# Performance work log

Hardware: AMD Instinct MI355X
Metric: run time of the kernel (lower is better)

Reference implementation:

```python
import jax, jax.numpy as jnp
import numpy as np


def _conv(x, w, b):
    # stride-2, pad-1 3x3 conv, NCHW/OIHW
    y = jax.lax.conv_general_dilated(x, w, (2, 2), [(1, 1), (1, 1)],
                                     dimension_numbers=('NCHW', 'OIHW', 'NCHW'))
    return y + b[None, :, None, None]


def _bn(x, g, b, eps=1e-5):
    # BatchNorm2d in training mode: batch statistics over (N, H, W)
    m = x.mean((0, 2, 3), keepdims=True)
    v = x.var((0, 2, 3), keepdims=True)
    return (x - m) * jax.lax.rsqrt(v + eps) * g[None, :, None, None] + b[None, :, None, None]


def setup_inputs() -> dict:
    key = jax.random.key(0)
    ks = iter(jax.random.split(key, 64))
    def rn(shape, scale):
        return jax.random.normal(next(ks), shape, jnp.float32) * scale
    d = {}
    d['img'] = jax.random.normal(next(ks), (64, 3, 128, 128), jnp.float32)
    d['qst'] = jax.random.normal(next(ks), (64, 11), jnp.float32)
    cin = 3
    for i in range(1, 5):
        d[f'cw{i}'] = rn((24, cin, 3, 3), 1.0 / np.sqrt(cin * 9))
        d[f'cb{i}'] = jnp.zeros((24,), jnp.float32)
        d[f'bg{i}'] = jnp.ones((24,), jnp.float32)
        d[f'bb{i}'] = jnp.zeros((24,), jnp.float32)
        cin = 24
    gdims = [63, 256, 256, 256]
    for i in range(1, 5):
        d[f'gw{i}'] = rn((gdims[i - 1], 256), 1.0 / np.sqrt(gdims[i - 1]))
        d[f'gb{i}'] = jnp.zeros((256,), jnp.float32)
    fdims = [(256, 256), (256, 256), (256, 10)]
    for i, (a, b) in enumerate(fdims, 1):
        d[f'fw{i}'] = rn((a, b), 1.0 / np.sqrt(a))
        d[f'fb{i}'] = jnp.zeros((b,), jnp.float32)
    return d


def reference(img, qst,
              cw1, cb1, bg1, bb1, cw2, cb2, bg2, bb2,
              cw3, cb3, bg3, bb3, cw4, cb4, bg4, bb4,
              gw1, gb1, gw2, gb2, gw3, gb3, gw4, gb4,
              fw1, fb1, fw2, fb2, fw3, fb3):
    x = img
    for cw, cb, bg, bb in ((cw1, cb1, bg1, bb1), (cw2, cb2, bg2, bb2),
                           (cw3, cb3, bg3, bb3), (cw4, cb4, bg4, bb4)):
        x = _bn(jax.nn.relu(_conv(x, cw, cb)), bg, bb)
    B, C, H, W = x.shape
    n = H * W  # number of objects (feature-map cells)
    o = x.reshape(B, C, n).transpose(0, 2, 1)  # [B, n, 24]
    idx = jnp.arange(n)
    coords = jnp.stack([idx // H, idx % W], axis=1).astype(x.dtype)  # [n, 2]
    o = jnp.concatenate([o, jnp.broadcast_to(coords, (B, n, 2))], axis=2)  # [B, n, 26]
    # First G layer fused over the pairwise concat cat([x_i, x_j, qst], -1) @ gw1:
    # x_i[b,a,c] = o[b,c], x_j[b,a,c] = o[b,a] -> split gw1 into the three blocks.
    Wi, Wj, Wq = gw1[:26], gw1[26:52], gw1[52:]
    h = jax.nn.relu((o @ Wi)[:, None, :, :]
                    + (o @ Wj)[:, :, None, :]
                    + (qst @ Wq + gb1)[:, None, None, :])  # [B, n, n, 256]
    h = jax.nn.relu(h @ gw2 + gb2)
    h = jax.nn.relu(h @ gw3 + gb3)
    h = jax.nn.relu(h @ gw4 + gb4)
    g = h.sum((1, 2))  # sum over all n*n pairs -> [B, 256]
    f = jax.nn.relu(g @ fw1 + fb1)
    f = jax.nn.relu(f @ fw2 + fb2)  # Dropout(0.5) is identity at inference
    return jax.nn.softmax(f @ fw3 + fb3, axis=-1)
```

## Files before the change

kernel.cpp:

```cpp
#include <hip/hip_runtime.h>
#include <hip/hip_bf16.h>

typedef __attribute__((ext_vector_type(8))) short bf16x8_t;
typedef __attribute__((ext_vector_type(4))) float f32x4_t;

__device__ __forceinline__ unsigned bfr(float x) {
  unsigned u = __builtin_bit_cast(unsigned, x);
  return (u + 0x7fffu + ((u >> 16) & 1u)) >> 16;
}
__device__ __forceinline__ unsigned pk2(float lo, float hi) {
  return bfr(lo) | (bfr(hi) << 16);
}

template<int CIN, int H, int COG, bool BNIN>
__global__ __launch_bounds__(256) void convk(
    const float* __restrict__ x, const float* __restrict__ wgt,
    const float* __restrict__ bias,
    const float* __restrict__ instats,
    const float* __restrict__ ing, const float* __restrict__ inb,
    float* __restrict__ y, float* __restrict__ stats)
{
  constexpr int W = H, HO = H / 2, WO = W / 2;
  constexpr int PXB = (COG == 1) ? 256 : 64;
  constexpr int OHS = PXB / WO;
  constexpr int SPB = HO / OHS;
  constexpr int NR = 2 * OHS + 1;
  constexpr int TW = W + 1;
  constexpr int NSTG = NR * W;
  constexpr int NCO = 24 / COG;

  __shared__ float tile[2][NR][TW];
  __shared__ float scb[CIN], shb[CIN];
  __shared__ float sred[24], sqd[24];

  const int tid = threadIdx.x;
  const int b = blockIdx.x / SPB;
  const int strip = blockIdx.x % SPB;
  const int oh0 = strip * OHS;
  const int lane = tid & 63;

  if (BNIN && tid < CIN) {
    const float cnt = 64.f * H * W;
    const float m = instats[tid] / cnt;
    const float v = instats[24 + tid] / cnt - m * m;
    const float s = rsqrtf(v + 1e-5f) * ing[tid];
    scb[tid] = s;
    shb[tid] = inb[tid] - m * s;
  }
  if (tid < 24) { sred[tid] = 0.f; sqd[tid] = 0.f; }
  for (int i = tid; i < 2 * NR; i += 256)
    tile[i / NR][i % NR][0] = 0.f;
  __syncthreads();

  const int px = (COG == 1) ? tid : lane;
  const int ow = px % WO;
  const int ohl = px / WO;
  const int oh = oh0 + ohl;
  const int cb = (COG == 1) ? 0
               : __builtin_amdgcn_readfirstlane(tid >> 6) * NCO;

  float acc[NCO];
  #pragma unroll
  for (int n = 0; n < NCO; ++n) acc[n] = bias[cb + n];

  {
    const float sc = BNIN ? scb[0] : 1.f, sh = BNIN ? shb[0] : 0.f;
    #pragma unroll
    for (int idx = tid; idx < NSTG; idx += 256) {
      const int c = idx % W, rl = idx / W;
      const int ih = oh0 * 2 - 1 + rl;
      float v = 0.f;
      if (ih >= 0)
        v = x[((size_t)(b * CIN + 0) * H + ih) * W + c] * sc + sh;
      tile[0][rl][c + 1] = v;
    }
  }
  __syncthreads();

  for (int ci = 0; ci < CIN; ++ci) {
    if (ci + 1 < CIN) {
      const float sc = BNIN ? scb[ci + 1] : 1.f, sh = BNIN ? shb[ci + 1] : 0.f;
      #pragma unroll
      for (int idx = tid; idx < NSTG; idx += 256) {
        const int c = idx % W, rl = idx / W;
        const int ih = oh0 * 2 - 1 + rl;
        float v = 0.f;
        if (ih >= 0)
          v = x[((size_t)(b * CIN + ci + 1) * H + ih) * W + c] * sc + sh;
        tile[(ci + 1) & 1][rl][c + 1] = v;
      }
    }
    float tp[9];
    #pragma unroll
    for (int r = 0; r < 3; ++r)
      #pragma unroll
      for (int s = 0; s < 3; ++s)
        tp[r * 3 + s] = tile[ci & 1][2 * ohl + r][2 * ow + s];
    #pragma unroll
    for (int n = 0; n < NCO; ++n) {
      const float* wp = wgt + (size_t)((cb + n) * CIN + ci) * 9;
      float a = acc[n];
      #pragma unroll
      for (int k = 0; k < 9; ++k) a += tp[k] * wp[k];
      acc[n] = a;
    }
    __syncthreads();
  }

  #pragma unroll
  for (int n = 0; n < NCO; ++n) {
    const float v = fmaxf(acc[n], 0.f);
    acc[n] = v;
    y[((size_t)(b * 24 + cb + n) * HO + oh) * WO + ow] = v;
  }
  #pragma unroll
  for (int n = 0; n < NCO; ++n) {
    float v = acc[n], q = v * v;
    #pragma unroll
    for (int d = 1; d < 64; d <<= 1) {
      v += __shfl_xor(v, d, 64);
      q += __shfl_xor(q, d, 64);
    }
    if (lane == 0) {
      atomicAdd(&sred[cb + n], v);
      atomicAdd(&sqd[cb + n], q);
    }
  }
  __syncthreads();
  if (tid < 24) {
    atomicAdd(&stats[tid], sred[tid]);
    atomicAdd(&stats[24 + tid], sqd[tid]);
  }
}

__global__ __launch_bounds__(256) void build_ab(
    const float* __restrict__ x4, const float* __restrict__ stats4,
    const float* __restrict__ g4, const float* __restrict__ b4,
    const float* __restrict__ gw1, const float* __restrict__ gb1,
    const float* __restrict__ qst,
    float* __restrict__ A, float* __restrict__ Bm, float* __restrict__ Cq)
{
  const int bp = blockIdx.x;
  const int b = bp >> 3, pg = bp & 7;
  const int t = threadIdx.x;
  __shared__ float o[8][26];
  if (t < 208) {
    const int r = t / 26, c = t % 26;
    if (c < 24) {
      const float m = stats4[c] * (1.f / 4096.f);
      const float v = stats4[24 + c] * (1.f / 4096.f) - m * m;
      const float sc = rsqrtf(v + 1e-5f) * g4[c];
      const float sh = b4[c] - m * sc;
      o[r][c] = x4[(size_t)(b * 24 + c) * 64 + pg * 8 + r] * sc + sh;
    } else if (c == 24) o[r][24] = (float)pg;
    else                o[r][25] = (float)r;
  }
  __syncthreads();
  float accA[8], accB[8];
  #pragma unroll
  for (int r = 0; r < 8; ++r) { accA[r] = 0.f; accB[r] = 0.f; }
  #pragma unroll
  for (int c = 0; c < 26; ++c) {
    const float wi = gw1[c * 256 + t];
    const float wj = gw1[(26 + c) * 256 + t];
    #pragma unroll
    for (int r = 0; r < 8; ++r) {
      accA[r] += o[r][c] * wi;
      accB[r] += o[r][c] * wj;
    }
  }
  #pragma unroll
  for (int r = 0; r < 8; ++r) {
    A[(size_t)(b * 64 + pg * 8 + r) * 256 + t]  = accA[r];
    Bm[(size_t)(b * 64 + pg * 8 + r) * 256 + t] = accB[r];
  }
  if (pg == 0) {
    float cqa = gb1[t];
    #pragma unroll
    for (int c = 0; c < 11; ++c)
      cqa += qst[b * 11 + c] * gw1[(52 + c) * 256 + t];
    Cq[b * 256 + t] = cqa;
  }
}

__global__ __launch_bounds__(256) void wt_convert_frag(
    const float* __restrict__ W2, const float* __restrict__ W3,
    const float* __restrict__ W4, unsigned short* __restrict__ wt)
{
  const int c = blockIdx.x;
  const int layer = c >> 3, ks = c & 7;
  const float* W = layer == 0 ? W2 : layer == 1 ? W3 : W4;
  const int t = threadIdx.x;
  #pragma unroll
  for (int q = 0; q < 4; ++q) {
    const int f = q * 256 + t;
    const int cg = f >> 8, a = (f >> 6) & 3, ln = f & 63;
    const int n = cg * 64 + a * 16 + (ln & 15);
    const int k0 = ks * 32 + (ln >> 4) * 8;
    float w[8];
    #pragma unroll
    for (int u = 0; u < 8; ++u) w[u] = W[(size_t)(k0 + u) * 256 + n];
    uint4 ov;
    ov.x = pk2(w[0], w[1]); ov.y = pk2(w[2], w[3]);
    ov.z = pk2(w[4], w[5]); ov.w = pk2(w[6], w[7]);
    *(uint4*)(wt + (size_t)c * 8192 + (size_t)f * 8) = ov;
  }
}

__global__ __launch_bounds__(256) void pair_mfma(
    const float* __restrict__ A, const float* __restrict__ Bm,
    const float* __restrict__ Cq,
    const unsigned short* __restrict__ wtall,
    const float* __restrict__ b2, const float* __restrict__ b3,
    const float* __restrict__ b4,
    float* __restrict__ Gpart)
{
  __shared__ __align__(16) unsigned short hsm[64 * 256];
  __shared__ __align__(16) unsigned short wbuf[2][8192];
  __shared__ float gpart[256];

  const int tid = threadIdx.x;
  int bid = blockIdx.x;
  bid = (bid & 7) * 512 + (bid >> 3);
  const int b = bid >> 6, local = bid & 63;
  const int lane = tid & 63, cg = tid >> 6;
  const int l15 = lane & 15, l4 = lane >> 4;
  char* hbase = (char*)hsm;

  {
    const int m = tid >> 2, seg = tid & 3;
    const float* Ar = A  + (size_t)(b * 64 + m) * 256 + seg * 64;
    const float* Br = Bm + (size_t)(b * 64 + local) * 256 + seg * 64;
    const float* Cr = Cq + (size_t)b * 256 + seg * 64;
    #pragma unroll
    for (int it = 0; it < 8; ++it) {
      const float4 a0 = *(const float4*)(Ar + it * 8);
      const float4 a1 = *(const float4*)(Ar + it * 8 + 4);
      const float4 b0 = *(const float4*)(Br + it * 8);
      const float4 b1 = *(const float4*)(Br + it * 8 + 4);
      const float4 c0 = *(const float4*)(Cr + it * 8);
      const float4 c1 = *(const float4*)(Cr + it * 8 + 4);
      uint4 pk;
      pk.x = pk2(fmaxf(a0.x + b0.x + c0.x, 0.f), fmaxf(a0.y + b0.y + c0.y, 0.f));
      pk.y = pk2(fmaxf(a0.z + b0.z + c0.z, 0.f), fmaxf(a0.w + b0.w + c0.w, 0.f));
      pk.z = pk2(fmaxf(a1.x + b1.x + c1.x, 0.f), fmaxf(a1.y + b1.y + c1.y, 0.f));
      pk.w = pk2(fmaxf(a1.z + b1.z + c1.z, 0.f), fmaxf(a1.w + b1.w + c1.w, 0.f));
      const int kb = seg * 128 + it * 16;
      *(uint4*)(hbase + (size_t)m * 512 + (kb ^ ((m & 7) << 4))) = pk;
    }
  }

  {
    const uint4* src = (const uint4*)wtall;
    uint4* dst = (uint4*)wbuf[0];
    #pragma unroll
    for (int q = 0; q < 4; ++q)
      dst[q * 256 + tid] = src[q * 256 + tid];
  }
  __syncthreads();

  const float* bs3[3] = {b2, b3, b4};

  for (int layer = 0; layer < 3; ++layer) {
    f32x4_t acc[4][4];
    #pragma unroll
    for (int a = 0; a < 4; ++a) {
      const float4 bv = *(const float4*)(bs3[layer] + cg * 64 + a * 16 + l4 * 4);
      #pragma unroll
      for (int t = 0; t < 4; ++t) {
        acc[a][t][0] = bv.x; acc[a][t][1] = bv.y;
        acc[a][t][2] = bv.z; acc[a][t][3] = bv.w;
      }
    }
    for (int ks = 0; ks < 8; ++ks) {
      const int c = layer * 8 + ks;
      uint4 p0, p1, p2, p3;
      if (c + 1 < 24) {
        const uint4* src = (const uint4*)wtall + (size_t)(c + 1) * 1024;
        p0 = src[0 * 256 + tid];
        p1 = src[1 * 256 + tid];
        p2 = src[2 * 256 + tid];
        p3 = src[3 * 256 + tid];
      }
      bf16x8_t bf[4];
      #pragma unroll
      for (int t = 0; t < 4; ++t) {
        const int row = t * 16 + l15;
        const int kb = ks * 64 + l4 * 16;
        bf[t] = *(const bf16x8_t*)(hbase + (size_t)row * 512 + (kb ^ ((row & 7) << 4)));
      }
      const unsigned short* wrd = wbuf[c & 1];
      #pragma unroll
      for (int a = 0; a < 4; ++a) {
        const bf16x8_t af = *(const bf16x8_t*)(wrd + ((size_t)(cg * 4 + a) * 64 + lane) * 8);
        #pragma unroll
        for (int t = 0; t < 4; ++t)
          acc[a][t] = __builtin_amdgcn_mfma_f32_16x16x32_bf16(af, bf[t], acc[a][t], 0, 0, 0);
      }
      if (c + 1 < 24) {
        uint4* wb = (uint4*)wbuf[(c + 1) & 1];
        wb[0 * 256 + tid] = p0;
        wb[1 * 256 + tid] = p1;
        wb[2 * 256 + tid] = p2;
        wb[3 * 256 + tid] = p3;
      }
      __syncthreads();
    }

    if (layer < 2) {
      #pragma unroll
      for (int a = 0; a < 4; ++a) {
        #pragma unroll
        for (int t = 0; t < 4; ++t) {
          const int row = t * 16 + l15;
          const int n0 = cg * 64 + a * 16 + l4 * 4;
          uint2 v;
          v.x = pk2(fmaxf(acc[a][t][0], 0.f), fmaxf(acc[a][t][1], 0.f));
          v.y = pk2(fmaxf(acc[a][t][2], 0.f), fmaxf(acc[a][t][3], 0.f));
          *(uint2*)(hbase + (size_t)row * 512 + ((n0 * 2) ^ ((row & 7) << 4))) = v;
        }
      }
      __syncthreads();
    } else {
      #pragma unroll
      for (int a = 0; a < 4; ++a) {
        f32x4_t s;
        s[0] = s[1] = s[2] = s[3] = 0.f;
        #pragma unroll
        for (int t = 0; t < 4; ++t) {
          s[0] += fmaxf(acc[a][t][0], 0.f);
          s[1] += fmaxf(acc[a][t][1], 0.f);
          s[2] += fmaxf(acc[a][t][2], 0.f);
          s[3] += fmaxf(acc[a][t][3], 0.f);
        }
        #pragma unroll
        for (int d = 1; d < 16; d <<= 1) {
          s[0] += __shfl_xor(s[0], d, 64);
          s[1] += __shfl_xor(s[1], d, 64);
          s[2] += __shfl_xor(s[2], d, 64);
          s[3] += __shfl_xor(s[3], d, 64);
        }
        if (l15 == 0)
          *(f32x4_t*)(&gpart[cg * 64 + a * 16 + l4 * 4]) = s;
      }
      __syncthreads();
      Gpart[(size_t)(b * 64 + local) * 256 + tid] = gpart[tid];
    }
  }
}

__global__ __launch_bounds__(256) void fnet(
    const float* __restrict__ Gpart,
    const float* __restrict__ fw1, const float* __restrict__ fb1,
    const float* __restrict__ fw2, const float* __restrict__ fb2,
    const float* __restrict__ fw3, const float* __restrict__ fb3,
    float* __restrict__ out)
{
  const int b = blockIdx.x, t = threadIdx.x;
  __shared__ float s0[256], s1[256], lg[10];
  float g = 0.f;
  for (int j = 0; j < 64; ++j)
    g += Gpart[(size_t)(b * 64 + j) * 256 + t];
  s0[t] = g;
  __syncthreads();
  float acc = fb1[t];
  for (int k = 0; k < 256; ++k) acc += s0[k] * fw1[k * 256 + t];
  s1[t] = fmaxf(acc, 0.f);
  __syncthreads();
  acc = fb2[t];
  for (int k = 0; k < 256; ++k) acc += s1[k] * fw2[k * 256 + t];
  s0[t] = fmaxf(acc, 0.f);
  __syncthreads();
  if (t < 10) {
    float a = fb3[t];
    for (int k = 0; k < 256; ++k) a += s0[k] * fw3[k * 10 + t];
    lg[t] = a;
  }
  __syncthreads();
  if (t == 0) {
    float m = lg[0];
    for (int c = 1; c < 10; ++c) m = fmaxf(m, lg[c]);
    float e[10], sum = 0.f;
    for (int c = 0; c < 10; ++c) { e[c] = expf(lg[c] - m); sum += e[c]; }
    const float inv = 1.f / sum;
    for (int c = 0; c < 10; ++c) out[b * 10 + c] = e[c] * inv;
  }
}

extern "C" void kernel_launch(void* const* d_in, const int* in_sizes, int n_in,
                              void* d_out, int out_size, void* d_ws, size_t ws_size,
                              hipStream_t stream)
{
  const float* img = (const float*)d_in[0];
  const float* qst = (const float*)d_in[1];
  const float* cw[4] = {(const float*)d_in[2],  (const float*)d_in[6],
                        (const float*)d_in[10], (const float*)d_in[14]};
  const float* cb[4] = {(const float*)d_in[3],  (const float*)d_in[7],
                        (const float*)d_in[11], (const float*)d_in[15]};
  const float* bg[4] = {(const float*)d_in[4],  (const float*)d_in[8],
                        (const float*)d_in[12], (const float*)d_in[16]};
  const float* bb[4] = {(const float*)d_in[5],  (const float*)d_in[9],
                        (const float*)d_in[13], (const float*)d_in[17]};
  const float* gw1 = (const float*)d_in[18];
  const float* gb1 = (const float*)d_in[19];
  const float* gw2 = (const float*)d_in[20];
  const float* gb2 = (const float*)d_in[21];
  const float* gw3 = (const float*)d_in[22];
  const float* gb3 = (const float*)d_in[23];
  const float* gw4 = (const float*)d_in[24];
  const float* gb4 = (const float*)d_in[25];
  const float* fw1 = (const float*)d_in[26];
  const float* fb1 = (const float*)d_in[27];
  const float* fw2 = (const float*)d_in[28];
  const float* fb2 = (const float*)d_in[29];
  const float* fw3 = (const float*)d_in[30];
  const float* fb3 = (const float*)d_in[31];
  float* out = (float*)d_out;

  float* ws    = (float*)d_ws;
  float* x1    = ws;
  float* x2    = x1 + 6291456;
  float* x3    = x2 + 1572864;
  float* x4    = x3 + 393216;
  float* Abuf  = x4 + 98304;
  float* Bbuf  = Abuf + 1048576;
  float* Cqb   = Bbuf + 1048576;
  float* Gpart = Cqb + 16384;
  float* stats = Gpart + 1048576;
  unsigned short* wtb = (unsigned short*)(stats + 192);

  hipMemsetAsync(stats, 0, 192 * sizeof(float), stream);

  wt_convert_frag<<<24, 256, 0, stream>>>(gw2, gw3, gw4, wtb);

  convk<3, 128, 1, false><<<1024, 256, 0, stream>>>(
      img, cw[0], cb[0], nullptr, nullptr, nullptr, x1, stats + 0);
  convk<24, 64, 4, true><<<1024, 256, 0, stream>>>(
      x1, cw[1], cb[1], stats + 0, bg[0], bb[0], x2, stats + 48);
  convk<24, 32, 4, true><<<256, 256, 0, stream>>>(
      x2, cw[2], cb[2], stats + 48, bg[1], bb[1], x3, stats + 96);
  convk<24, 16, 4, true><<<64, 256, 0, stream>>>(
      x3, cw[3], cb[3], stats + 96, bg[2], bb[2], x4, stats + 144);

  build_ab<<<512, 256, 0, stream>>>(x4, stats + 144, bg[3], bb[3], gw1,
                                    gb1, qst, Abuf, Bbuf, Cqb);

  pair_mfma<<<4096, 256, 0, stream>>>(Abuf, Bbuf, Cqb, wtb, gb2, gb3, gb4,
                                      Gpart);
  fnet<<<64, 256, 0, stream>>>(Gpart, fw1, fb1, fw2, fb2, fw3, fb3, out);
}
```

Before: 556.0 us.

## Load pair-MLP weight fragments straight into registers and ping-pong activation LDS

The pair MLP kernel no longer stages weight chunks through a double-buffered LDS ring with a barrier per k-step. Each wave now loads its whole layer's bf16 weight fragments from global (L2) into registers up front. Activations alternate between two LDS buffers so each layer can write its output without overwriting its input. The stats memset is folded into the weight conversion kernel to drop one launch. The cost is a large register footprint (32 bf16x8 fragments plus 16 accumulators), which launch_bounds(256,2) must accommodate, so spilling or lower occupancy is possible.

Result: faster. 539.6 us (-2.9%).

```diff
diff --git a/kernel.cpp b/kernel.cpp
--- a/kernel.cpp
+++ b/kernel.cpp
@@ -185,12 +185,14 @@
 
 __global__ __launch_bounds__(256) void wt_convert_frag(
     const float* __restrict__ W2, const float* __restrict__ W3,
-    const float* __restrict__ W4, unsigned short* __restrict__ wt)
+    const float* __restrict__ W4, unsigned short* __restrict__ wt,
+    float* __restrict__ stats)
 {
   const int c = blockIdx.x;
+  const int t = threadIdx.x;
+  if (c == 0 && t < 192) stats[t] = 0.f;
   const int layer = c >> 3, ks = c & 7;
   const float* W = layer == 0 ? W2 : layer == 1 ? W3 : W4;
-  const int t = threadIdx.x;
   #pragma unroll
   for (int q = 0; q < 4; ++q) {
     const int f = q * 256 + t;
@@ -207,7 +209,7 @@
   }
 }
 
-__global__ __launch_bounds__(256) void pair_mfma(
+__global__ __launch_bounds__(256, 2) void pair_mfma(
     const float* __restrict__ A, const float* __restrict__ Bm,
     const float* __restrict__ Cq,
     const unsigned short* __restrict__ wtall,
@@ -215,8 +217,7 @@
     const float* __restrict__ b4,
     float* __restrict__ Gpart)
 {
-  __shared__ __align__(16) unsigned short hsm[64 * 256];
-  __shared__ __align__(16) unsigned short wbuf[2][8192];
+  __shared__ __align__(16) unsigned short hsm[2][64 * 256];
   __shared__ float gpart[256];
 
   const int tid = threadIdx.x;
@@ -225,9 +226,9 @@
   const int b = bid >> 6, local = bid & 63;
   const int lane = tid & 63, cg = tid >> 6;
   const int l15 = lane & 15, l4 = lane >> 4;
-  char* hbase = (char*)hsm;
 
   {
+    char* h0 = (char*)hsm[0];
     const int m = tid >> 2, seg = tid & 3;
     const float* Ar = A  + (size_t)(b * 64 + m) * 256 + seg * 64;
     const float* Br = Bm + (size_t)(b * 64 + local) * 256 + seg * 64;
@@ -246,22 +247,29 @@
       pk.z = pk2(fmaxf(a1.x + b1.x + c1.x, 0.f), fmaxf(a1.y + b1.y + c1.y, 0.f));
       pk.w = pk2(fmaxf(a1.z + b1.z + c1.z, 0.f), fmaxf(a1.w + b1.w + c1.w, 0.f));
       const int kb = seg * 128 + it * 16;
-      *(uint4*)(hbase + (size_t)m * 512 + (kb ^ ((m & 7) << 4))) = pk;
-    }
-  }
-
-  {
-    const uint4* src = (const uint4*)wtall;
-    uint4* dst = (uint4*)wbuf[0];
-    #pragma unroll
-    for (int q = 0; q < 4; ++q)
-      dst[q * 256 + tid] = src[q * 256 + tid];
+      *(uint4*)(h0 + (size_t)m * 512 + (kb ^ ((m & 7) << 4))) = pk;
+    }
   }
   __syncthreads();
 
   const float* bs3[3] = {b2, b3, b4};
 
+  #pragma unroll
   for (int layer = 0; layer < 3; ++layer) {
+    const char* hread = (const char*)hsm[layer & 1];
+    char* hwrite = (char*)hsm[(layer & 1) ^ 1];
+
+    bf16x8_t af[8][4];
+    {
+      const unsigned short* wl =
+          wtall + (size_t)layer * 65536 + ((size_t)(cg * 4) * 64 + lane) * 8;
+      #pragma unroll
+      for (int ks = 0; ks < 8; ++ks)
+        #pragma unroll
+        for (int a = 0; a < 4; ++a)
+          af[ks][a] = *(const bf16x8_t*)(wl + (size_t)ks * 8192 + a * 512);
+    }
+
     f32x4_t acc[4][4];
     #pragma unroll
     for (int a = 0; a < 4; ++a) {
@@ -272,39 +280,22 @@
         acc[a][t][2] = bv.z; acc[a][t][3] = bv.w;
       }
     }
+
+    #pragma unroll
     for (int ks = 0; ks < 8; ++ks) {
-      const int c = layer * 8 + ks;
-      uint4 p0, p1, p2, p3;
-      if (c + 1 < 24) {
-        const uint4* src = (const uint4*)wtall + (size_t)(c + 1) * 1024;
-        p0 = src[0 * 256 + tid];
-        p1 = src[1 * 256 + tid];
-        p2 = src[2 * 256 + tid];
-        p3 = src[3 * 256 + tid];
-      }
       bf16x8_t bf[4];
       #pragma unroll
       for (int t = 0; t < 4; ++t) {
         const int row = t * 16 + l15;
         const int kb = ks * 64 + l4 * 16;
-        bf[t] = *(const bf16x8_t*)(hbase + (size_t)row * 512 + (kb ^ ((row & 7) << 4)));
+        bf[t] = *(const bf16x8_t*)(hread + (size_t)row * 512 + (kb ^ ((row & 7) << 4)));
       }
-      const unsigned short* wrd = wbuf[c & 1];
-      #pragma unroll
-      for (int a = 0; a < 4; ++a) {
-        const bf16x8_t af = *(const bf16x8_t*)(wrd + ((size_t)(cg * 4 + a) * 64 + lane) * 8);
+      #pragma unroll
+      for (int a = 0; a < 4; ++a)
         #pragma unroll
         for (int t = 0; t < 4; ++t)
-          acc[a][t] = __builtin_amdgcn_mfma_f32_16x16x32_bf16(af, bf[t], acc[a][t], 0, 0, 0);
-      }
-      if (c + 1 < 24) {
-        uint4* wb = (uint4*)wbuf[(c + 1) & 1];
-        wb[0 * 256 + tid] = p0;
-        wb[1 * 256 + tid] = p1;
-        wb[2 * 256 + tid] = p2;
-        wb[3 * 256 + tid] = p3;
-      }
-      __syncthreads();
+          acc[a][t] = __builtin_amdgcn_mfma_f32_16x16x32_bf16(
+              af[ks][a], bf[t], acc[a][t], 0, 0, 0);
     }
 
     if (layer < 2) {
@@ -317,7 +308,7 @@
           uint2 v;
           v.x = pk2(fmaxf(acc[a][t][0], 0.f), fmaxf(acc[a][t][1], 0.f));
           v.y = pk2(fmaxf(acc[a][t][2], 0.f), fmaxf(acc[a][t][3], 0.f));
-          *(uint2*)(hbase + (size_t)row * 512 + ((n0 * 2) ^ ((row & 7) << 4))) = v;
+          *(uint2*)(hwrite + (size_t)row * 512 + ((n0 * 2) ^ ((row & 7) << 4))) = v;
         }
       }
       __syncthreads();
@@ -429,9 +420,7 @@
   float* stats = Gpart + 1048576;
   unsigned short* wtb = (unsigned short*)(stats + 192);
 
-  hipMemsetAsync(stats, 0, 192 * sizeof(float), stream);
-
-  wt_convert_frag<<<24, 256, 0, stream>>>(gw2, gw3, gw4, wtb);
+  wt_convert_frag<<<24, 256, 0, stream>>>(gw2, gw3, gw4, wtb, stats);
 
   convk<3, 128, 1, false><<<1024, 256, 0, stream>>>(
       img, cw[0], cb[0], nullptr, nullptr, nullptr, x1, stats + 0);
```
